# Performance work log

Measured on AMD Instinct MI355X. Metric: run time of the kernel, lower is better.

The kernel has to match this reference:

```python
import jax, jax.numpy as jnp
import numpy as np

D_DEPTH = 41   # arange(4.0, 45.0, 1.0)
CAM_C = 64
IMG_H, IMG_W = 512, 1408
DOWNS = 16
FH, FW = IMG_H // DOWNS, IMG_W // DOWNS  # 32, 88
NX, NY, NZ = 200, 200, 1                 # gen_dx_bx of the fixed bounds
DX = np.array([0.25, 0.25, 20.0], np.float32)
BX = np.array([-25.0 + 0.125, 0.0 + 0.125, 0.0], np.float32)  # row0 + row2/2


def _frustum():
    # [D, FH, FW, 3] with (pixel_x, pixel_y, depth)
    ds = np.arange(4.0, 45.0, 1.0, dtype=np.float32).reshape(-1, 1, 1)
    xs = np.linspace(0, IMG_W - 1, FW, dtype=np.float32).reshape(1, 1, FW)
    ys = np.linspace(0, IMG_H - 1, FH, dtype=np.float32).reshape(1, FH, 1)
    ds, xs, ys = np.broadcast_arrays(
        np.broadcast_to(ds, (D_DEPTH, FH, FW)), xs, ys)[0:1] + list(
        np.broadcast_arrays(xs, ys, ds)[:2]) if False else (
        np.broadcast_to(ds, (D_DEPTH, FH, FW)),
        np.broadcast_to(xs, (D_DEPTH, FH, FW)),
        np.broadcast_to(ys, (D_DEPTH, FH, FW)))
    return np.stack([xs, ys, ds], axis=-1)


def setup_inputs() -> dict:
    key = jax.random.key(0)
    k1, k2, k3 = jax.random.split(key, 3)
    B = 4
    feat = jax.random.normal(k1, (B, 256, FH, FW), jnp.float32)
    # realistic pinhole intrinsics with per-sample focal jitter
    fx = 0.5 * IMG_W / np.tan(np.deg2rad(35.0))
    s = 0.9 + 0.2 * jax.random.uniform(k2, (B,), jnp.float32)
    intrins = (jnp.zeros((B, 3, 3), jnp.float32)
               .at[:, 0, 0].set(fx * s)
               .at[:, 1, 1].set(fx * s)
               .at[:, 0, 2].set(IMG_W / 2.0)
               .at[:, 1, 2].set(IMG_H / 2.0)
               .at[:, 2, 2].set(1.0))
    w_depth = jax.random.normal(k3, (D_DEPTH + CAM_C, 256), jnp.float32) * 0.05
    b_depth = jnp.zeros((D_DEPTH + CAM_C,), jnp.float32)
    return {"feat": feat, "intrins": intrins, "w_depth": w_depth, "b_depth": b_depth}


def reference(feat, intrins, w_depth, b_depth):
    B = feat.shape[0]
    # depthnet 1x1 conv: 256 -> D + C
    x = jnp.einsum('bchw,oc->bohw', feat, w_depth) + b_depth[None, :, None, None]
    depth = jax.nn.softmax(x[:, :D_DEPTH], axis=1)               # [B,D,fH,fW]
    # lift: depth distribution outer-product with context features
    lifted = depth[:, None] * x[:, D_DEPTH:, None]               # [B,C,D,fH,fW]
    feats = lifted.transpose(0, 2, 3, 4, 1).reshape(-1, CAM_C)   # [B*D*fH*fW, C]

    # geometry: unproject frustum pixels through inverse intrinsics
    fr = jnp.asarray(_frustum())                                 # [D,fH,fW,3]
    pix = jnp.concatenate([fr[..., :2] * fr[..., 2:3], fr[..., 2:3]], axis=-1)
    inv = jnp.linalg.inv(intrins)                                # [B,3,3]
    pts = jnp.einsum('bij,dhwj->bdhwi', inv, pix)                # [B,D,fH,fW,3]

    dx = jnp.asarray(DX); bx = jnp.asarray(BX)
    geom = ((pts - (bx - dx / 2.0)) / dx).astype(jnp.int32)      # trunc like .long()
    geom = geom.reshape(-1, 3)
    n_per = geom.shape[0] // B
    bix = jnp.repeat(jnp.arange(B, dtype=jnp.int32), n_per)
    gx, gy, gz = geom[:, 0], geom[:, 1], geom[:, 2]
    kept = ((gx >= 0) & (gx < NX) & (gy >= 0) & (gy < NY)
            & (gz >= 0) & (gz < NZ))
    ranks = gx * (NY * NZ * B) + gy * (NZ * B) + gz * B + bix
    nseg = NX * NY * NZ * B
    seg = jnp.where(kept, ranks, nseg)  # out-of-range -> dummy bucket
    # sort+cumsum+diff dedup over ranks == segment sum per voxel
    sums = jax.ops.segment_sum(feats, seg, num_segments=nseg + 1)[:nseg]
    grid = sums.reshape(NX, NY, NZ, B, CAM_C).transpose(3, 4, 2, 0, 1)  # B,C,Z,X,Y
    bev = grid.reshape(B, CAM_C * NZ, NX, NY)  # cat of Z slices along channels
    return bev[:, :, :196, :]
```

## Files before the change

### kernel.cpp

```cpp
#include <hip/hip_runtime.h>
#include <math.h>

#define B_      4
#define CIN     256
#define FH_     32
#define FW_     88
#define HWN     (FH_*FW_)
#define DND     41
#define CC      64
#define NO      105
#define NXg     200
#define NYg     200
#define NXOUT   196
#define PLANE   (NXOUT*NYg)
#define XPAD    112
#define NPOS    (B_*HWN)

#define GX0     71
#define GXW     58
#define GYW     29
#define WCELLS  (GXW*GYW)
#define WSG_F   (B_*WCELLS*CC)

__global__ void zero_ws_kernel(float4* __restrict__ p) {
  int i = blockIdx.x*blockDim.x + threadIdx.x;
  if (i < WSG_F/4) p[i] = make_float4(0.f,0.f,0.f,0.f);
}

#define BM 32
#define KCH 64
#define LDO 68
__global__ __launch_bounds__(256) void gemm_kernel(
    const float* __restrict__ feat, const float* __restrict__ wd,
    const float* __restrict__ bd, float* __restrict__ xbuf)
{
  __shared__ float __attribute__((aligned(16))) ft[KCH*BM];
  __shared__ float __attribute__((aligned(16))) Wl[KCH*LDO];

  const int t     = threadIdx.x;
  const int mtile = blockIdx.x;
  const int o0    = blockIdx.y * 64;
  const int b     = mtile / 88;
  const int hw0   = (mtile - b*88) * BM;
  const float* featB = feat + (size_t)b*CIN*HWN + hw0;

  const int tm = t & 15;
  const int to = t >> 4;
  float acc[2][4] = {{0,0,0,0},{0,0,0,0}};

  for (int k0 = 0; k0 < CIN; k0 += KCH) {
    #pragma unroll
    for (int r = 0; r < 2; ++r) {
      int idx = r*256 + t;
      int c = idx >> 3, m4 = (idx & 7) * 4;
      *reinterpret_cast<float4*>(&ft[c*BM + m4]) =
        *reinterpret_cast<const float4*>(&featB[(size_t)(k0+c)*HWN + m4]);
    }
    #pragma unroll
    for (int pass = 0; pass < 4; ++pass) {
      int o  = t & 63;
      int c4 = ((t >> 6) + pass*4) * 4;
      int og = o0 + o;
      float4 v = make_float4(0.f,0.f,0.f,0.f);
      if (og < NO) v = *reinterpret_cast<const float4*>(&wd[(size_t)og*CIN + k0 + c4]);
      Wl[(c4+0)*LDO + o] = v.x;
      Wl[(c4+1)*LDO + o] = v.y;
      Wl[(c4+2)*LDO + o] = v.z;
      Wl[(c4+3)*LDO + o] = v.w;
    }
    __syncthreads();
    #pragma unroll 8
    for (int c = 0; c < KCH; ++c) {
      float2 fm = *reinterpret_cast<const float2*>(&ft[c*BM + tm*2]);
      float4 wv = *reinterpret_cast<const float4*>(&Wl[c*LDO + to*4]);
      acc[0][0] += fm.x*wv.x; acc[0][1] += fm.x*wv.y; acc[0][2] += fm.x*wv.z; acc[0][3] += fm.x*wv.w;
      acc[1][0] += fm.y*wv.x; acc[1][1] += fm.y*wv.y; acc[1][2] += fm.y*wv.z; acc[1][3] += fm.y*wv.w;
    }
    __syncthreads();
  }

  const int obase = o0 + to*4;
  float bv[4];
  #pragma unroll
  for (int j = 0; j < 4; ++j) bv[j] = (obase + j < NO) ? bd[obase + j] : 0.f;
  const int pos0 = mtile*BM + tm*2;
  #pragma unroll
  for (int i = 0; i < 2; ++i) {
    int pos = pos0 + i;
    float* row = xbuf + (size_t)pos*XPAD + obase;
    if (obase + 3 < NO) {
      float4 v = make_float4(acc[i][0]+bv[0], acc[i][1]+bv[1], acc[i][2]+bv[2], acc[i][3]+bv[3]);
      *reinterpret_cast<float4*>(row) = v;
    } else {
      #pragma unroll
      for (int j = 0; j < 4; ++j)
        if (obase + j < NO) row[j] = acc[i][j] + bv[j];
    }
  }
}

__global__ __launch_bounds__(256) void scatter_kernel(
    const float* __restrict__ xbuf, const float* __restrict__ intr,
    float* __restrict__ wsg)
{
  const int t    = threadIdx.x;
  const int lane = t & 63;
  const int pos  = blockIdx.x*4 + (t >> 6);
  const int b    = pos / HWN;
  const int rem  = pos - b*HWN;
  const int h    = rem / FW_;
  const int w    = rem - h*FW_;

  const float fv  = intr[b*9 + 0];
  const float cxv = intr[b*9 + 2];
  const float cyv = intr[b*9 + 5];
  const float rf  = __fdiv_rn(1.0f, fv);
  const float i02 = -__fmul_rn(rf, cxv);
  const float i12 = -__fmul_rn(rf, cyv);

  const float xw = (float)((double)w * (1407.0/87.0));
  const float yh = (float)((double)h * (511.0/31.0));

  int cells[6];
  bool any = false;
  #pragma unroll
  for (int d = 0; d < 6; ++d) {
    float dval = 4.0f + (float)d;
    float px = __fadd_rn(__fmul_rn(rf, __fmul_rn(xw, dval)), __fmul_rn(i02, dval));
    float py = __fadd_rn(__fmul_rn(rf, __fmul_rn(yh, dval)), __fmul_rn(i12, dval));
    int gx = (int)__fdiv_rn(__fadd_rn(px, 25.0f), 0.25f);
    int gy = (int)__fdiv_rn(py, 0.25f);
    int c = -1;
    if (gx >= 0 && gx < NXOUT && gy >= 0 && gy < NYg) {
      int gxw = gx - GX0;
      if (gxw >= 0 && gxw < GXW && gy < GYW) c = gxw*GYW + gy;
    }
    cells[d] = c;
    any = any || (c >= 0);
  }
  if (!any) return;

  const float* xr = xbuf + (size_t)pos*XPAD;
  float logit = (lane < DND) ? xr[lane] : -1e30f;
  float mx = logit;
  #pragma unroll
  for (int s = 1; s < 64; s <<= 1) mx = fmaxf(mx, __shfl_xor(mx, s));
  float e = (lane < DND) ? expf(logit - mx) : 0.f;
  float den = e;
  #pragma unroll
  for (int s = 1; s < 64; s <<= 1) den += __shfl_xor(den, s);
  const float rden = 1.0f / den;

  const float xc = xr[DND + lane];
  float* wsB = wsg + (size_t)b*WCELLS*CC;

  int curCell = -2; float wacc = 0.f;
  #pragma unroll
  for (int d = 0; d < 6; ++d) {
    int cd = cells[d];
    float pd = __shfl(e, d) * rden;
    if (cd != curCell) {
      if (curCell >= 0) atomicAdd(wsB + (size_t)curCell*CC + lane, wacc * xc);
      curCell = cd; wacc = 0.f;
    }
    if (cd >= 0) wacc += pd;
  }
  if (curCell >= 0) atomicAdd(wsB + (size_t)curCell*CC + lane, wacc * xc);
}

__global__ void transpose_kernel(const float* __restrict__ wsg, float* __restrict__ out) {
  int tid = blockIdx.x*blockDim.x + threadIdx.x;
  if (tid >= B_*CC*NXOUT*(NYg/4)) return;
  int gy4 = tid % (NYg/4);
  int r   = tid / (NYg/4);
  int gx  = r % NXOUT; r /= NXOUT;
  int c   = r % CC;
  int b   = r / CC;
  float4 v = make_float4(0.f,0.f,0.f,0.f);
  int gxw = gx - GX0;
  int gy0 = gy4*4;
  if (gxw >= 0 && gxw < GXW && gy0 < GYW) {
    const float* base = wsg + ((size_t)((b*GXW + gxw)*GYW))*CC + c;
    v.x = base[(size_t)(gy0+0)*CC];
    if (gy0+1 < GYW) v.y = base[(size_t)(gy0+1)*CC];
    if (gy0+2 < GYW) v.z = base[(size_t)(gy0+2)*CC];
    if (gy0+3 < GYW) v.w = base[(size_t)(gy0+3)*CC];
  }
  reinterpret_cast<float4*>(out)[tid] = v;
}

extern "C" void kernel_launch(void* const* d_in, const int* in_sizes, int n_in,
                              void* d_out, int out_size, void* d_ws, size_t ws_size,
                              hipStream_t stream) {
  const float* feat = (const float*)d_in[0];
  const float* intr = (const float*)d_in[1];
  const float* wd   = (const float*)d_in[2];
  const float* bd   = (const float*)d_in[3];
  float* out  = (float*)d_out;
  float* xbuf = (float*)d_ws;
  float* wsg  = (float*)d_ws + (size_t)NPOS*XPAD;

  zero_ws_kernel<<<dim3((WSG_F/4 + 255)/256), dim3(256), 0, stream>>>((float4*)wsg);
  gemm_kernel<<<dim3(352, 2), dim3(256), 0, stream>>>(feat, wd, bd, xbuf);
  scatter_kernel<<<dim3(NPOS/4), dim3(256), 0, stream>>>(xbuf, intr, wsg);
  transpose_kernel<<<dim3(B_*CC*NXOUT*(NYg/4)/256), dim3(256), 0, stream>>>(wsg, out);
}
```

Baseline: 114.2 us.

## Fuse depthnet GEMM with softmax-lift scatter and skip fully culled tiles

```diff
diff --git a/kernel.cpp b/kernel.cpp
--- a/kernel.cpp
+++ b/kernel.cpp
@@ -9,11 +9,9 @@
 #define DND     41
 #define CC      64
 #define NO      105
-#define NXg     200
+#define NXOUT   196
 #define NYg     200
-#define NXOUT   196
 #define PLANE   (NXOUT*NYg)
-#define XPAD    112
 #define NPOS    (B_*HWN)
 
 #define GX0     71
@@ -27,89 +25,30 @@
   if (i < WSG_F/4) p[i] = make_float4(0.f,0.f,0.f,0.f);
 }
 
-#define BM 32
-#define KCH 64
-#define LDO 68
-__global__ __launch_bounds__(256) void gemm_kernel(
-    const float* __restrict__ feat, const float* __restrict__ wd,
-    const float* __restrict__ bd, float* __restrict__ xbuf)
+#define BM   32
+#define KCH  64
+__global__ __launch_bounds__(256) void fused_kernel(
+    const float* __restrict__ feat, const float* __restrict__ intr,
+    const float* __restrict__ wd, const float* __restrict__ bd,
+    float* __restrict__ wsg)
 {
-  __shared__ float __attribute__((aligned(16))) ft[KCH*BM];
-  __shared__ float __attribute__((aligned(16))) Wl[KCH*LDO];
+  __shared__ float __attribute__((aligned(16))) smem[10240];
+  __shared__ int   geomLds[BM*6];
+  __shared__ int   posAny[BM];
+  __shared__ int   anyKept;
+
+  float* ft = smem;
+  float* Wl = smem + 2048;
+  float* xs = smem;
 
   const int t     = threadIdx.x;
   const int mtile = blockIdx.x;
-  const int o0    = blockIdx.y * 64;
   const int b     = mtile / 88;
   const int hw0   = (mtile - b*88) * BM;
-  const float* featB = feat + (size_t)b*CIN*HWN + hw0;
-
-  const int tm = t & 15;
-  const int to = t >> 4;
-  float acc[2][4] = {{0,0,0,0},{0,0,0,0}};
-
-  for (int k0 = 0; k0 < CIN; k0 += KCH) {
-    #pragma unroll
-    for (int r = 0; r < 2; ++r) {
-      int idx = r*256 + t;
-      int c = idx >> 3, m4 = (idx & 7) * 4;
-      *reinterpret_cast<float4*>(&ft[c*BM + m4]) =
-        *reinterpret_cast<const float4*>(&featB[(size_t)(k0+c)*HWN + m4]);
-    }
-    #pragma unroll
-    for (int pass = 0; pass < 4; ++pass) {
-      int o  = t & 63;
-      int c4 = ((t >> 6) + pass*4) * 4;
-      int og = o0 + o;
-      float4 v = make_float4(0.f,0.f,0.f,0.f);
-      if (og < NO) v = *reinterpret_cast<const float4*>(&wd[(size_t)og*CIN + k0 + c4]);
-      Wl[(c4+0)*LDO + o] = v.x;
-      Wl[(c4+1)*LDO + o] = v.y;
-      Wl[(c4+2)*LDO + o] = v.z;
-      Wl[(c4+3)*LDO + o] = v.w;
-    }
-    __syncthreads();
-    #pragma unroll 8
-    for (int c = 0; c < KCH; ++c) {
-      float2 fm = *reinterpret_cast<const float2*>(&ft[c*BM + tm*2]);
-      float4 wv = *reinterpret_cast<const float4*>(&Wl[c*LDO + to*4]);
-      acc[0][0] += fm.x*wv.x; acc[0][1] += fm.x*wv.y; acc[0][2] += fm.x*wv.z; acc[0][3] += fm.x*wv.w;
-      acc[1][0] += fm.y*wv.x; acc[1][1] += fm.y*wv.y; acc[1][2] += fm.y*wv.z; acc[1][3] += fm.y*wv.w;
-    }
-    __syncthreads();
-  }
-
-  const int obase = o0 + to*4;
-  float bv[4];
-  #pragma unroll
-  for (int j = 0; j < 4; ++j) bv[j] = (obase + j < NO) ? bd[obase + j] : 0.f;
-  const int pos0 = mtile*BM + tm*2;
-  #pragma unroll
-  for (int i = 0; i < 2; ++i) {
-    int pos = pos0 + i;
-    float* row = xbuf + (size_t)pos*XPAD + obase;
-    if (obase + 3 < NO) {
-      float4 v = make_float4(acc[i][0]+bv[0], acc[i][1]+bv[1], acc[i][2]+bv[2], acc[i][3]+bv[3]);
-      *reinterpret_cast<float4*>(row) = v;
-    } else {
-      #pragma unroll
-      for (int j = 0; j < 4; ++j)
-        if (obase + j < NO) row[j] = acc[i][j] + bv[j];
-    }
-  }
-}
-
-__global__ __launch_bounds__(256) void scatter_kernel(
-    const float* __restrict__ xbuf, const float* __restrict__ intr,
-    float* __restrict__ wsg)
-{
-  const int t    = threadIdx.x;
-  const int lane = t & 63;
-  const int pos  = blockIdx.x*4 + (t >> 6);
-  const int b    = pos / HWN;
-  const int rem  = pos - b*HWN;
-  const int h    = rem / FW_;
-  const int w    = rem - h*FW_;
+
+  if (t < BM) posAny[t] = 0;
+  if (t == 0) anyKept = 0;
+  __syncthreads();
 
   const float fv  = intr[b*9 + 0];
   const float cxv = intr[b*9 + 2];
@@ -118,54 +57,116 @@
   const float i02 = -__fmul_rn(rf, cxv);
   const float i12 = -__fmul_rn(rf, cyv);
 
-  const float xw = (float)((double)w * (1407.0/87.0));
-  const float yh = (float)((double)h * (511.0/31.0));
-
-  int cells[6];
-  bool any = false;
-  #pragma unroll
-  for (int d = 0; d < 6; ++d) {
+  if (t < BM*6) {
+    int m = t / 6;
+    int d = t - m*6;
+    int hw = hw0 + m;
+    int h  = hw / FW_;
+    int w  = hw - h*FW_;
+    float xw = (float)((double)w * (1407.0/87.0));
+    float yh = (float)((double)h * (511.0/31.0));
     float dval = 4.0f + (float)d;
     float px = __fadd_rn(__fmul_rn(rf, __fmul_rn(xw, dval)), __fmul_rn(i02, dval));
     float py = __fadd_rn(__fmul_rn(rf, __fmul_rn(yh, dval)), __fmul_rn(i12, dval));
     int gx = (int)__fdiv_rn(__fadd_rn(px, 25.0f), 0.25f);
     int gy = (int)__fdiv_rn(py, 0.25f);
-    int c = -1;
+    int cell = -1;
     if (gx >= 0 && gx < NXOUT && gy >= 0 && gy < NYg) {
       int gxw = gx - GX0;
-      if (gxw >= 0 && gxw < GXW && gy < GYW) c = gxw*GYW + gy;
-    }
-    cells[d] = c;
-    any = any || (c >= 0);
-  }
-  if (!any) return;
-
-  const float* xr = xbuf + (size_t)pos*XPAD;
-  float logit = (lane < DND) ? xr[lane] : -1e30f;
-  float mx = logit;
+      if (gxw >= 0 && gxw < GXW && gy < GYW) cell = gxw*GYW + gy;
+    }
+    geomLds[t] = cell;
+    if (cell >= 0) { posAny[m] = 1; anyKept = 1; }
+  }
+  __syncthreads();
+  if (!anyKept) return;
+
+  const float* featB = feat + (size_t)b*CIN*HWN + hw0;
+  const int tm = t & 15;
+  const int to = t >> 4;
+  float acc[2][8];
   #pragma unroll
-  for (int s = 1; s < 64; s <<= 1) mx = fmaxf(mx, __shfl_xor(mx, s));
-  float e = (lane < DND) ? expf(logit - mx) : 0.f;
-  float den = e;
+  for (int i = 0; i < 2; ++i)
+    #pragma unroll
+    for (int j = 0; j < 8; ++j) acc[i][j] = 0.f;
+
+  for (int k0 = 0; k0 < CIN; k0 += KCH) {
+    #pragma unroll
+    for (int r = 0; r < 2; ++r) {
+      int idx = r*256 + t;
+      int c = idx >> 3, m4 = (idx & 7) * 4;
+      *reinterpret_cast<float4*>(&ft[c*BM + m4]) =
+        *reinterpret_cast<const float4*>(&featB[(size_t)(k0+c)*HWN + m4]);
+    }
+    #pragma unroll
+    for (int pass = 0; pass < 8; ++pass) {
+      int idx = pass*256 + t;
+      int o   = idx & 127;
+      int c4  = (idx >> 7) * 4;
+      float4 v = make_float4(0.f,0.f,0.f,0.f);
+      if (o < NO) v = *reinterpret_cast<const float4*>(&wd[(size_t)o*CIN + k0 + c4]);
+      Wl[(c4+0)*128 + o] = v.x;
+      Wl[(c4+1)*128 + o] = v.y;
+      Wl[(c4+2)*128 + o] = v.z;
+      Wl[(c4+3)*128 + o] = v.w;
+    }
+    __syncthreads();
+    #pragma unroll 8
+    for (int c = 0; c < KCH; ++c) {
+      float2 fm = *reinterpret_cast<const float2*>(&ft[c*BM + tm*2]);
+      float4 wa = *reinterpret_cast<const float4*>(&Wl[c*128 + to*8]);
+      float4 wb = *reinterpret_cast<const float4*>(&Wl[c*128 + to*8 + 4]);
+      acc[0][0] += fm.x*wa.x; acc[0][1] += fm.x*wa.y; acc[0][2] += fm.x*wa.z; acc[0][3] += fm.x*wa.w;
+      acc[0][4] += fm.x*wb.x; acc[0][5] += fm.x*wb.y; acc[0][6] += fm.x*wb.z; acc[0][7] += fm.x*wb.w;
+      acc[1][0] += fm.y*wa.x; acc[1][1] += fm.y*wa.y; acc[1][2] += fm.y*wa.z; acc[1][3] += fm.y*wa.w;
+      acc[1][4] += fm.y*wb.x; acc[1][5] += fm.y*wb.y; acc[1][6] += fm.y*wb.z; acc[1][7] += fm.y*wb.w;
+    }
+    __syncthreads();
+  }
+
+  const int obase = to*8;
   #pragma unroll
-  for (int s = 1; s < 64; s <<= 1) den += __shfl_xor(den, s);
-  const float rden = 1.0f / den;
-
-  const float xc = xr[DND + lane];
+  for (int i = 0; i < 2; ++i) {
+    int m = tm*2 + i;
+    #pragma unroll
+    for (int j = 0; j < 8; ++j) {
+      int o = obase + j;
+      if (o < NO) xs[m*112 + o] = acc[i][j] + bd[o];
+    }
+  }
+  __syncthreads();
+
+  const int wv   = t >> 6;
+  const int lane = t & 63;
   float* wsB = wsg + (size_t)b*WCELLS*CC;
-
-  int curCell = -2; float wacc = 0.f;
-  #pragma unroll
-  for (int d = 0; d < 6; ++d) {
-    int cd = cells[d];
-    float pd = __shfl(e, d) * rden;
-    if (cd != curCell) {
-      if (curCell >= 0) atomicAdd(wsB + (size_t)curCell*CC + lane, wacc * xc);
-      curCell = cd; wacc = 0.f;
-    }
-    if (cd >= 0) wacc += pd;
-  }
-  if (curCell >= 0) atomicAdd(wsB + (size_t)curCell*CC + lane, wacc * xc);
+  for (int q = 0; q < 8; ++q) {
+    int mp = wv*8 + q;
+    if (!posAny[mp]) continue;
+    const float* xr = &xs[mp*112];
+    float logit = (lane < DND) ? xr[lane] : -1e30f;
+    float mx = logit;
+    #pragma unroll
+    for (int s = 1; s < 64; s <<= 1) mx = fmaxf(mx, __shfl_xor(mx, s));
+    float e = (lane < DND) ? expf(logit - mx) : 0.f;
+    float den = e;
+    #pragma unroll
+    for (int s = 1; s < 64; s <<= 1) den += __shfl_xor(den, s);
+    const float rden = 1.0f / den;
+    const float xc = xr[DND + lane];
+
+    int curCell = -2; float wacc = 0.f;
+    #pragma unroll
+    for (int d = 0; d < 6; ++d) {
+      int cd = geomLds[mp*6 + d];
+      float pd = __shfl(e, d) * rden;
+      if (cd != curCell) {
+        if (curCell >= 0) atomicAdd(wsB + (size_t)curCell*CC + lane, wacc * xc);
+        curCell = cd; wacc = 0.f;
+      }
+      if (cd >= 0) wacc += pd;
+    }
+    if (curCell >= 0) atomicAdd(wsB + (size_t)curCell*CC + lane, wacc * xc);
+  }
 }
 
 __global__ void transpose_kernel(const float* __restrict__ wsg, float* __restrict__ out) {
@@ -196,12 +197,10 @@
   const float* intr = (const float*)d_in[1];
   const float* wd   = (const float*)d_in[2];
   const float* bd   = (const float*)d_in[3];
-  float* out  = (float*)d_out;
-  float* xbuf = (float*)d_ws;
-  float* wsg  = (float*)d_ws + (size_t)NPOS*XPAD;
+  float* out = (float*)d_out;
+  float* wsg = (float*)d_ws;
 
   zero_ws_kernel<<<dim3((WSG_F/4 + 255)/256), dim3(256), 0, stream>>>((float4*)wsg);
-  gemm_kernel<<<dim3(352, 2), dim3(256), 0, stream>>>(feat, wd, bd, xbuf);
-  scatter_kernel<<<dim3(NPOS/4), dim3(256), 0, stream>>>(xbuf, intr, wsg);
+  fused_kernel<<<dim3(352), dim3(256), 0, stream>>>(feat, intr, wd, bd, wsg);
   transpose_kernel<<<dim3(B_*CC*NXOUT*(NYg/4)/256), dim3(256), 0, stream>>>(wsg, out);
 }
```

New measurement: 115.8 us. Within noise of the previous version (+1.4%).
